# Performance work log

Measured on AMD Instinct MI355X. Metric: run time of the kernel, lower is better.

Reference implementation:

```python
import jax, jax.numpy as jnp
import numpy as np

LOG2 = 0.6931471805599453

def logcosh(x):
    # numerically stable log(cosh(x)) = |x| + log1p(exp(-2|x|)) - log(2)
    ax = jnp.abs(x)
    return ax + jnp.log1p(jnp.exp(-2.0 * ax)) - LOG2

def setup_inputs() -> dict:
    key = jax.random.key(0)
    k1, k2, k3 = jax.random.split(key, 3)
    B, N, G, F = 16384, 1024, 256, 16  # batch, n_sites, n_symm, alpha_symm
    # each row of perms is a valid permutation of [0, N)
    perms = jax.vmap(lambda k: jax.random.permutation(k, N))(jax.random.split(k1, G)).astype(jnp.int32)
    x = jax.random.normal(k2, (B, N), dtype=jnp.float32)
    W = jax.random.normal(k3, (N, F), dtype=jnp.float32) * 0.1  # kernel_init = normal(0.1)
    b = jnp.zeros((F,), dtype=jnp.float32)
    v_bias = jnp.zeros((1,), dtype=jnp.float32)
    return {"x": x, "W": W, "b": b, "v_bias": v_bias, "perms": perms}

def reference(x, W, b, v_bias, perms):
    # scan over group permutations: gather x by perm, matmul, bias, logcosh, sum
    def f(carry, perm):
        y = x[..., perm] @ W + b          # [B, F]
        return carry + jnp.sum(logcosh(y), axis=-1), None
    y0 = jnp.zeros(x.shape[:-1], dtype=x.dtype)
    y_out, _ = jax.lax.scan(f, y0, perms)
    y_out = y_out + v_bias[0] * jnp.sum(x, axis=-1)
    return y_out
```

## Files before the change

### kernel.cpp

```cpp
#include <hip/hip_runtime.h>
#include <math.h>

typedef __bf16 bf16x8 __attribute__((ext_vector_type(8)));
typedef float f32x4 __attribute__((ext_vector_type(4)));


__device__ __forceinline__ unsigned short f2bf(float f) {
    unsigned int u = __float_as_uint(f);
    u += 0x7FFFu + ((u >> 16) & 1u);
    return (unsigned short)(u >> 16);
}

__device__ __forceinline__ float logcosh_fast(float v) {
    float a = fabsf(v);
    float t = __expf(-2.0f * a);
    return a + (__logf(1.0f + t) - 0.6931471805599453f);
}

template <int CTRL>
__device__ __forceinline__ float dppadd(float x) {
    int y = __builtin_amdgcn_update_dpp(0, __float_as_int(x), CTRL, 0xf, 0xf, true);
    return x + __int_as_float(y);
}

__device__ __forceinline__ void gload_lds16(const void* g, void* l) {
    __builtin_amdgcn_global_load_lds(
        (__attribute__((address_space(1))) void*)(void*)g,
        (__attribute__((address_space(3))) void*)l, 16, 0, 0);
}

#define SBAR()  __builtin_amdgcn_s_barrier()
#define SCHED() __builtin_amdgcn_sched_barrier(0)

__global__ __launch_bounds__(256) void k_invert(const int* __restrict__ perms,
                                                int* __restrict__ inv) {
    int t = blockIdx.x * 256 + threadIdx.x;
    int g = t >> 10, n = t & 1023;
    inv[(g << 10) + perms[t]] = n;
}

__global__ __launch_bounds__(256) void k_build_bt(const float* __restrict__ W,
                                                  const int* __restrict__ inv,
                                                  unsigned short* __restrict__ bT) {
    int j = blockIdx.x;
    int g = j >> 4, f = j & 15;
    const int* invg = inv + (g << 10);
    size_t rowbase = (size_t)j << 10;
#pragma unroll
    for (int i = 0; i < 4; ++i) {
        int k = (i << 8) + threadIdx.x;
        int n = invg[k];
        bT[rowbase + k] = f2bf(W[(n << 4) + f]);
    }
}

__global__ __launch_bounds__(256) void k_convert(const float* __restrict__ x,
                                                 const float* __restrict__ vb,
                                                 unsigned short* __restrict__ xb,
                                                 float* __restrict__ out) {
    int row = blockIdx.x, tid = threadIdx.x;
    size_t base = ((size_t)row << 10) + (tid << 2);
    float4 v = *reinterpret_cast<const float4*>(x + base);
    ushort4 h;
    h.x = f2bf(v.x); h.y = f2bf(v.y); h.z = f2bf(v.z); h.w = f2bf(v.w);
    *reinterpret_cast<ushort4*>(xb + base) = h;
    float s = v.x + v.y + v.z + v.w;
#pragma unroll
    for (int off = 32; off > 0; off >>= 1) s += __shfl_down(s, off);
    __shared__ float ls[4];
    if ((tid & 63) == 0) ls[tid >> 6] = s;
    __syncthreads();
    if (tid == 0) out[row] = vb[0] * (ls[0] + ls[1] + ls[2] + ls[3]);
}


#define MFMA_QUAD(MH, NH)                                                        \
    _Pragma("unroll") for (int m_ = 0; m_ < 4; ++m_)                             \
    _Pragma("unroll") for (int n_ = 0; n_ < 2; ++n_)                             \
    _Pragma("unroll") for (int kk_ = 0; kk_ < 2; ++kk_)                          \
        acc[(MH) * 4 + m_][(NH) * 2 + n_] =                                      \
            __builtin_amdgcn_mfma_f32_16x16x32_bf16(                             \
                aF[(MH) * 4 + m_][kk_], bF[(NH) * 2 + n_][kk_],                  \
                acc[(MH) * 4 + m_][(NH) * 2 + n_], 0, 0, 0);

__global__ __launch_bounds__(512) void k_gemm(const unsigned short* __restrict__ xb,
                                              const unsigned short* __restrict__ bT,
                                              const float* __restrict__ bias,
                                              float* __restrict__ partial, int B) {
    __shared__ unsigned short As[2][256 * 64];
    __shared__ unsigned short Bs[2][256 * 64];

    const int tid = threadIdx.x;
    const int lane = tid & 63;
    const int wv = tid >> 6;
    const int wm = wv >> 2;
    const int wn = wv & 3;
    const int lr = lane & 15;
    const int lk = lane >> 4;

    const int fid = blockIdx.y * gridDim.x + blockIdx.x;
    const int cpx = (gridDim.x * gridDim.y) >> 3;
    const int swz = (fid & 7) * cpx + (fid >> 3);
    const int cbx = swz & 15;
    const int row0 = (swz >> 4) << 8;
    const int j0 = cbx << 8;

    const unsigned short* xbase = xb + ((size_t)row0 << 10);
    const unsigned short* bbase = bT + ((size_t)j0 << 10);

    const int aRow = (wm * 128 + lr) * 64;
    const int bRow = (wn * 64 + lr) * 64;
    const int po0 = (lk ^ (lr & 7)) * 8;
    const int po1 = ((4 + lk) ^ (lr & 7)) * 8;

    auto stage_half = [&](unsigned short* dst, const unsigned short* src, int h) {
#pragma unroll
        for (int j = 0; j < 2; ++j) {
            int c0 = (h * 128 + j * 64) * 8;
            int cc = c0 + tid;
            int r = cc >> 3;
            int cs = (cc & 7) ^ (r & 7);
            gload_lds16(src + (((size_t)r) << 10) + (cs << 3),
                        dst + ((c0 + wv * 64) << 3));
        }
    };
    auto stage_slot = [&](int tile, int part) {
        if (tile > 15) return;
        int p = tile & 1;
        const unsigned short* src = (part < 2 ? xbase : bbase) + (tile << 6);
        unsigned short* dst = (part < 2 ? &As[p][0] : &Bs[p][0]);
        stage_half(dst, src, part & 1);
    };

    f32x4 acc[8][4];
#pragma unroll
    for (int m = 0; m < 8; ++m)
#pragma unroll
        for (int n = 0; n < 4; ++n)
            acc[m][n] = {0.f, 0.f, 0.f, 0.f};

    stage_slot(0, 0); stage_slot(0, 1); stage_slot(0, 2); stage_slot(0, 3);
    stage_slot(1, 0);
    asm volatile("s_waitcnt vmcnt(2)" ::: "memory");
    SCHED();
    SBAR();

    for (int tt = 0; tt < 8; ++tt) {
        const int t = tt * 2;

        auto half_iter = [&](const unsigned short* Ap, const unsigned short* Bp,
                             int st1, int st4, int vm) {
            bf16x8 aF[8][2], bF[4][2];

#pragma unroll
            for (int m = 0; m < 4; ++m) {
                aF[m][0] = *reinterpret_cast<const bf16x8*>(Ap + aRow + po0 + m * 1024);
                aF[m][1] = *reinterpret_cast<const bf16x8*>(Ap + aRow + po1 + m * 1024);
            }
#pragma unroll
            for (int n = 0; n < 2; ++n) {
                bF[n][0] = *reinterpret_cast<const bf16x8*>(Bp + bRow + po0 + n * 1024);
                bF[n][1] = *reinterpret_cast<const bf16x8*>(Bp + bRow + po1 + n * 1024);
            }
            stage_slot(st1, 1);
            SCHED();
            SBAR();
            asm volatile("s_waitcnt lgkmcnt(0)" ::: "memory");
            SCHED();
            __builtin_amdgcn_s_setprio(1);
            MFMA_QUAD(0, 0)
            __builtin_amdgcn_s_setprio(0);
            SCHED();
            SBAR();

#pragma unroll
            for (int m = 4; m < 8; ++m) {
                aF[m][0] = *reinterpret_cast<const bf16x8*>(Ap + aRow + po0 + m * 1024);
                aF[m][1] = *reinterpret_cast<const bf16x8*>(Ap + aRow + po1 + m * 1024);
            }
            SCHED();
#pragma unroll
            for (int n = 2; n < 4; ++n) {
                bF[n][0] = *reinterpret_cast<const bf16x8*>(Bp + bRow + po0 + n * 1024);
                bF[n][1] = *reinterpret_cast<const bf16x8*>(Bp + bRow + po1 + n * 1024);
            }
            stage_slot(st1, 2);
            SCHED();
            SBAR();
            asm volatile("s_waitcnt lgkmcnt(4)" ::: "memory");
            SCHED();
            __builtin_amdgcn_s_setprio(1);
            MFMA_QUAD(1, 0)
            __builtin_amdgcn_s_setprio(0);
            SCHED();
            SBAR();

            stage_slot(st1, 3);
            SCHED();
            SBAR();
            asm volatile("s_waitcnt lgkmcnt(0)" ::: "memory");
            SCHED();
            __builtin_amdgcn_s_setprio(1);
            MFMA_QUAD(0, 1)
            __builtin_amdgcn_s_setprio(0);
            SCHED();
            SBAR();

            stage_slot(st4, 0);
            SCHED();
            SBAR();
            __builtin_amdgcn_s_setprio(1);
            MFMA_QUAD(1, 1)
            __builtin_amdgcn_s_setprio(0);
            SCHED();
            if (vm == 2)      { asm volatile("s_waitcnt vmcnt(2)" ::: "memory"); }
            else if (vm == 0) { asm volatile("s_waitcnt vmcnt(0)" ::: "memory"); }
            SCHED();
            SBAR();
        };

        half_iter(As[0], Bs[0], t + 1, t + 2, (tt < 7) ? 2 : 0);
        half_iter(As[1], Bs[1], t + 2, t + 3, (tt < 7) ? 2 : -1);
    }

    float* rowsum = (float*)&As[0][0];
    const float bv = bias[lr];
#pragma unroll
    for (int m = 0; m < 8; ++m) {
#pragma unroll
        for (int r = 0; r < 4; ++r) {
            float s = 0.f;
#pragma unroll
            for (int n = 0; n < 4; ++n) s += logcosh_fast(acc[m][n][r] + bv);
            s = dppadd<0x111>(s);
            s = dppadd<0x112>(s);
            s = dppadd<0x114>(s);
            s = dppadd<0x118>(s);
            if (lr == 15)
                rowsum[wn * 256 + wm * 128 + m * 16 + lk * 4 + r] = s;
        }
    }
    __syncthreads();
    if (tid < 256) {
        float s = rowsum[tid] + rowsum[256 + tid] + rowsum[512 + tid] + rowsum[768 + tid];
        partial[(size_t)cbx * B + row0 + tid] = s;
    }
}

__global__ __launch_bounds__(256) void k_final(const float* __restrict__ partial,
                                               float* __restrict__ out, int ncb, int B) {
    int b = blockIdx.x * 256 + threadIdx.x;
    float s = out[b];
    for (int c = 0; c < ncb; ++c) s += partial[(size_t)c * B + b];
    out[b] = s;
}

extern "C" void kernel_launch(void* const* d_in, const int* in_sizes, int n_in,
                              void* d_out, int out_size, void* d_ws, size_t ws_size,
                              hipStream_t stream) {
    const float* x      = (const float*)d_in[0];
    const float* W      = (const float*)d_in[1];
    const float* bias   = (const float*)d_in[2];
    const float* v_bias = (const float*)d_in[3];
    const int*   perms  = (const int*)d_in[4];
    float* out = (float*)d_out;

    const int N  = 1024;
    const int B  = in_sizes[0] / N;
    const int G  = in_sizes[4] / N;
    const int GF = G * 16;
    const int NCB = GF / 256;

    char* w = (char*)d_ws;
    unsigned short* xb = (unsigned short*)w;
    unsigned short* bT = (unsigned short*)(w + (size_t)B * N * 2);
    int* inv = (int*)(w + (size_t)B * N * 2 + (size_t)GF * N * 2);
    float* partial = (float*)(w + (size_t)B * N * 2 + (size_t)GF * N * 2
                              + (size_t)G * N * 4);

    k_invert<<<G * N / 256, 256, 0, stream>>>(perms, inv);
    k_build_bt<<<GF, 256, 0, stream>>>(W, inv, bT);
    k_convert<<<B, 256, 0, stream>>>(x, v_bias, xb, out);
    k_gemm<<<dim3(NCB, B / 256), 512, 0, stream>>>(xb, bT, bias, partial, B);
    k_final<<<B / 256, 256, 0, stream>>>(partial, out, NCB, B);
}
```

Baseline: 204.4 us.

## Restructure GEMM pipeline to prefetch next tile's fragments and reorder LDS staging

Replaces the lambda-based half-iteration with a templated tile4 step. It loads the next tile's first A/B register fragments at the end of the current tile, so the LDS reads overlap the last MFMA quadrant instead of stalling at the start. The staging schedule changes from A-ahead to a B-then-A order, and the prologue now preloads two A tiles. The launch bounds now ask for 2 blocks per CU, which pressures registers given the larger live fragment set and may cause spills. The risk is a race on LDS buffer reuse, since A is staged into the buffer currently being read.

```diff
diff --git a/kernel.cpp b/kernel.cpp
--- a/kernel.cpp
+++ b/kernel.cpp
@@ -83,10 +83,92 @@
                 aF[(MH) * 4 + m_][kk_], bF[(NH) * 2 + n_][kk_],                  \
                 acc[(MH) * 4 + m_][(NH) * 2 + n_], 0, 0, 0);
 
-__global__ __launch_bounds__(512) void k_gemm(const unsigned short* __restrict__ xb,
-                                              const unsigned short* __restrict__ bT,
-                                              const float* __restrict__ bias,
-                                              float* __restrict__ partial, int B) {
+__device__ __forceinline__ void stage_half(unsigned short* dst,
+                                           const unsigned short* src, int h,
+                                           int tid, int wv) {
+#pragma unroll
+    for (int j = 0; j < 2; ++j) {
+        int c0 = (h * 128 + j * 64) * 8;
+        int cc = c0 + tid;
+        int r = cc >> 3;
+        int cs = (cc & 7) ^ (r & 7);
+        gload_lds16(src + (((size_t)r) << 10) + (cs << 3),
+                    dst + ((c0 + wv * 64) << 3));
+    }
+}
+
+template <int VM, bool STB, bool STA, bool RDN>
+__device__ __forceinline__ void tile4(
+    const unsigned short* Ap, const unsigned short* Bp,
+    unsigned short* BsQ, unsigned short* AsP,
+    const unsigned short* bsrc, const unsigned short* xsrc,
+    const unsigned short* Aq, const unsigned short* Bq,
+    bf16x8 (&aF)[8][2], bf16x8 (&bF)[4][2], f32x4 (&acc)[8][4],
+    int aRow, int bRow, int po0, int po1, int tid, int wv) {
+#pragma unroll
+    for (int m = 4; m < 8; ++m) {
+        aF[m][0] = *reinterpret_cast<const bf16x8*>(Ap + aRow + po0 + m * 1024);
+        aF[m][1] = *reinterpret_cast<const bf16x8*>(Ap + aRow + po1 + m * 1024);
+    }
+    if (STB) stage_half(BsQ, bsrc, 0, tid, wv);
+    SCHED(); SBAR();
+    asm volatile("s_waitcnt lgkmcnt(8)" ::: "memory");
+    SCHED();
+    __builtin_amdgcn_s_setprio(1);
+    MFMA_QUAD(0, 0)
+    __builtin_amdgcn_s_setprio(0);
+    SCHED(); SBAR();
+
+#pragma unroll
+    for (int n = 2; n < 4; ++n) {
+        bF[n][0] = *reinterpret_cast<const bf16x8*>(Bp + bRow + po0 + n * 1024);
+        bF[n][1] = *reinterpret_cast<const bf16x8*>(Bp + bRow + po1 + n * 1024);
+    }
+    if (STB) stage_half(BsQ, bsrc, 1, tid, wv);
+    SCHED(); SBAR();
+    asm volatile("s_waitcnt lgkmcnt(4)" ::: "memory");
+    SCHED();
+    __builtin_amdgcn_s_setprio(1);
+    MFMA_QUAD(1, 0)
+    __builtin_amdgcn_s_setprio(0);
+    SCHED(); SBAR();
+
+    if (STA) stage_half(AsP, xsrc, 0, tid, wv);
+    SCHED(); SBAR();
+    asm volatile("s_waitcnt lgkmcnt(0)" ::: "memory");
+    SCHED();
+    __builtin_amdgcn_s_setprio(1);
+    MFMA_QUAD(0, 1)
+    __builtin_amdgcn_s_setprio(0);
+    SCHED();
+    if (VM == 2)      { asm volatile("s_waitcnt vmcnt(2)" ::: "memory"); }
+    else if (VM == 0) { asm volatile("s_waitcnt vmcnt(0)" ::: "memory"); }
+    SCHED(); SBAR();
+
+    if (RDN) {
+#pragma unroll
+        for (int m = 0; m < 4; ++m) {
+            aF[m][0] = *reinterpret_cast<const bf16x8*>(Aq + aRow + po0 + m * 1024);
+            aF[m][1] = *reinterpret_cast<const bf16x8*>(Aq + aRow + po1 + m * 1024);
+        }
+#pragma unroll
+        for (int n = 0; n < 2; ++n) {
+            bF[n][0] = *reinterpret_cast<const bf16x8*>(Bq + bRow + po0 + n * 1024);
+            bF[n][1] = *reinterpret_cast<const bf16x8*>(Bq + bRow + po1 + n * 1024);
+        }
+    }
+    if (STA) stage_half(AsP, xsrc, 1, tid, wv);
+    SCHED(); SBAR();
+    __builtin_amdgcn_s_setprio(1);
+    MFMA_QUAD(1, 1)
+    __builtin_amdgcn_s_setprio(0);
+    SCHED(); SBAR();
+}
+
+__global__ __launch_bounds__(512, 2) void k_gemm(const unsigned short* __restrict__ xb,
+                                                 const unsigned short* __restrict__ bT,
+                                                 const float* __restrict__ bias,
+                                                 float* __restrict__ partial, int B) {
     __shared__ unsigned short As[2][256 * 64];
     __shared__ unsigned short Bs[2][256 * 64];
 
@@ -113,25 +195,6 @@
     const int po0 = (lk ^ (lr & 7)) * 8;
     const int po1 = ((4 + lk) ^ (lr & 7)) * 8;
 
-    auto stage_half = [&](unsigned short* dst, const unsigned short* src, int h) {
-#pragma unroll
-        for (int j = 0; j < 2; ++j) {
-            int c0 = (h * 128 + j * 64) * 8;
-            int cc = c0 + tid;
-            int r = cc >> 3;
-            int cs = (cc & 7) ^ (r & 7);
-            gload_lds16(src + (((size_t)r) << 10) + (cs << 3),
-                        dst + ((c0 + wv * 64) << 3));
-        }
-    };
-    auto stage_slot = [&](int tile, int part) {
-        if (tile > 15) return;
-        int p = tile & 1;
-        const unsigned short* src = (part < 2 ? xbase : bbase) + (tile << 6);
-        unsigned short* dst = (part < 2 ? &As[p][0] : &Bs[p][0]);
-        stage_half(dst, src, part & 1);
-    };
-
     f32x4 acc[8][4];
 #pragma unroll
     for (int m = 0; m < 8; ++m)
@@ -139,89 +202,47 @@
         for (int n = 0; n < 4; ++n)
             acc[m][n] = {0.f, 0.f, 0.f, 0.f};
 
-    stage_slot(0, 0); stage_slot(0, 1); stage_slot(0, 2); stage_slot(0, 3);
-    stage_slot(1, 0);
-    asm volatile("s_waitcnt vmcnt(2)" ::: "memory");
-    SCHED();
-    SBAR();
-
-    for (int tt = 0; tt < 8; ++tt) {
-        const int t = tt * 2;
-
-        auto half_iter = [&](const unsigned short* Ap, const unsigned short* Bp,
-                             int st1, int st4, int vm) {
-            bf16x8 aF[8][2], bF[4][2];
-
-#pragma unroll
-            for (int m = 0; m < 4; ++m) {
-                aF[m][0] = *reinterpret_cast<const bf16x8*>(Ap + aRow + po0 + m * 1024);
-                aF[m][1] = *reinterpret_cast<const bf16x8*>(Ap + aRow + po1 + m * 1024);
-            }
-#pragma unroll
-            for (int n = 0; n < 2; ++n) {
-                bF[n][0] = *reinterpret_cast<const bf16x8*>(Bp + bRow + po0 + n * 1024);
-                bF[n][1] = *reinterpret_cast<const bf16x8*>(Bp + bRow + po1 + n * 1024);
-            }
-            stage_slot(st1, 1);
-            SCHED();
-            SBAR();
-            asm volatile("s_waitcnt lgkmcnt(0)" ::: "memory");
-            SCHED();
-            __builtin_amdgcn_s_setprio(1);
-            MFMA_QUAD(0, 0)
-            __builtin_amdgcn_s_setprio(0);
-            SCHED();
-            SBAR();
-
-#pragma unroll
-            for (int m = 4; m < 8; ++m) {
-                aF[m][0] = *reinterpret_cast<const bf16x8*>(Ap + aRow + po0 + m * 1024);
-                aF[m][1] = *reinterpret_cast<const bf16x8*>(Ap + aRow + po1 + m * 1024);
-            }
-            SCHED();
-#pragma unroll
-            for (int n = 2; n < 4; ++n) {
-                bF[n][0] = *reinterpret_cast<const bf16x8*>(Bp + bRow + po0 + n * 1024);
-                bF[n][1] = *reinterpret_cast<const bf16x8*>(Bp + bRow + po1 + n * 1024);
-            }
-            stage_slot(st1, 2);
-            SCHED();
-            SBAR();
-            asm volatile("s_waitcnt lgkmcnt(4)" ::: "memory");
-            SCHED();
-            __builtin_amdgcn_s_setprio(1);
-            MFMA_QUAD(1, 0)
-            __builtin_amdgcn_s_setprio(0);
-            SCHED();
-            SBAR();
-
-            stage_slot(st1, 3);
-            SCHED();
-            SBAR();
-            asm volatile("s_waitcnt lgkmcnt(0)" ::: "memory");
-            SCHED();
-            __builtin_amdgcn_s_setprio(1);
-            MFMA_QUAD(0, 1)
-            __builtin_amdgcn_s_setprio(0);
-            SCHED();
-            SBAR();
-
-            stage_slot(st4, 0);
-            SCHED();
-            SBAR();
-            __builtin_amdgcn_s_setprio(1);
-            MFMA_QUAD(1, 1)
-            __builtin_amdgcn_s_setprio(0);
-            SCHED();
-            if (vm == 2)      { asm volatile("s_waitcnt vmcnt(2)" ::: "memory"); }
-            else if (vm == 0) { asm volatile("s_waitcnt vmcnt(0)" ::: "memory"); }
-            SCHED();
-            SBAR();
-        };
-
-        half_iter(As[0], Bs[0], t + 1, t + 2, (tt < 7) ? 2 : 0);
-        half_iter(As[1], Bs[1], t + 2, t + 3, (tt < 7) ? 2 : -1);
-    }
+    bf16x8 aF[8][2], bF[4][2];
+
+    stage_half(&As[0][0], xbase, 0, tid, wv);
+    stage_half(&As[0][0], xbase, 1, tid, wv);
+    stage_half(&Bs[0][0], bbase, 0, tid, wv);
+    stage_half(&Bs[0][0], bbase, 1, tid, wv);
+    stage_half(&As[1][0], xbase + 64, 0, tid, wv);
+    stage_half(&As[1][0], xbase + 64, 1, tid, wv);
+    asm volatile("s_waitcnt vmcnt(4)" ::: "memory");
+    SCHED(); SBAR();
+#pragma unroll
+    for (int m = 0; m < 4; ++m) {
+        aF[m][0] = *reinterpret_cast<const bf16x8*>(&As[0][0] + aRow + po0 + m * 1024);
+        aF[m][1] = *reinterpret_cast<const bf16x8*>(&As[0][0] + aRow + po1 + m * 1024);
+    }
+#pragma unroll
+    for (int n = 0; n < 2; ++n) {
+        bF[n][0] = *reinterpret_cast<const bf16x8*>(&Bs[0][0] + bRow + po0 + n * 1024);
+        bF[n][1] = *reinterpret_cast<const bf16x8*>(&Bs[0][0] + bRow + po1 + n * 1024);
+    }
+    SCHED();
+
+    for (int tt = 0; tt < 7; ++tt) {
+        const int t0 = tt * 2;
+        tile4<2, true, true, true>(&As[0][0], &Bs[0][0], &Bs[1][0], &As[0][0],
+                                   bbase + ((t0 + 1) << 6), xbase + ((t0 + 2) << 6),
+                                   &As[1][0], &Bs[1][0],
+                                   aF, bF, acc, aRow, bRow, po0, po1, tid, wv);
+        tile4<2, true, true, true>(&As[1][0], &Bs[1][0], &Bs[0][0], &As[1][0],
+                                   bbase + ((t0 + 2) << 6), xbase + ((t0 + 3) << 6),
+                                   &As[0][0], &Bs[0][0],
+                                   aF, bF, acc, aRow, bRow, po0, po1, tid, wv);
+    }
+    tile4<0, true, false, true>(&As[0][0], &Bs[0][0], &Bs[1][0], &As[0][0],
+                                bbase + (15 << 6), xbase,
+                                &As[1][0], &Bs[1][0],
+                                aF, bF, acc, aRow, bRow, po0, po1, tid, wv);
+    tile4<-1, false, false, false>(&As[1][0], &Bs[1][0], &Bs[0][0], &As[1][0],
+                                   bbase, xbase,
+                                   &As[0][0], &Bs[0][0],
+                                   aF, bF, acc, aRow, bRow, po0, po1, tid, wv);
 
     float* rowsum = (float*)&As[0][0];
     const float bv = bias[lr];
```

Measured after the change: 250.9 us. +22.7%, slower.

## Restructure GEMM main loop into per-row MFMA pipeline with two-tile-ahead prefetch

Applied to the files above, without the earlier changes.

Replaces the quad-based half-iteration schedule with a tile iteration that loads all B fragments up front and streams A fragments one M-row at a time, interleaving LDS reads with MFMAs. Both double-buffer slots are now staged before the loop, and each tile refills its own slot two tiles ahead after its last LDS read, which cuts the number of barriers per tile. Launch bounds also request two blocks per CU. The tighter register budget from that hint could force spills of the large accumulator array, and LDS use may prevent the second block from fitting anyway.

```diff
diff --git a/kernel.cpp b/kernel.cpp
--- a/kernel.cpp
+++ b/kernel.cpp
@@ -74,19 +74,86 @@
 }
 
 
-#define MFMA_QUAD(MH, NH)                                                        \
-    _Pragma("unroll") for (int m_ = 0; m_ < 4; ++m_)                             \
-    _Pragma("unroll") for (int n_ = 0; n_ < 2; ++n_)                             \
-    _Pragma("unroll") for (int kk_ = 0; kk_ < 2; ++kk_)                          \
-        acc[(MH) * 4 + m_][(NH) * 2 + n_] =                                      \
-            __builtin_amdgcn_mfma_f32_16x16x32_bf16(                             \
-                aF[(MH) * 4 + m_][kk_], bF[(NH) * 2 + n_][kk_],                  \
-                acc[(MH) * 4 + m_][(NH) * 2 + n_], 0, 0, 0);
-
-__global__ __launch_bounds__(512) void k_gemm(const unsigned short* __restrict__ xb,
-                                              const unsigned short* __restrict__ bT,
-                                              const float* __restrict__ bias,
-                                              float* __restrict__ partial, int B) {
+#define MFMA_M(MM)                                                               \
+    _Pragma("unroll") for (int k_ = 0; k_ < 2; ++k_)                             \
+    _Pragma("unroll") for (int n_ = 0; n_ < 4; ++n_)                             \
+        acc[MM][n_] = __builtin_amdgcn_mfma_f32_16x16x32_bf16(                   \
+            aF[MM][k_], bF[n_][k_], acc[MM][n_], 0, 0, 0);
+
+__device__ __forceinline__ void stage_half(unsigned short* dst,
+                                           const unsigned short* src, int h,
+                                           int tid, int wv) {
+#pragma unroll
+    for (int j = 0; j < 2; ++j) {
+        int c0 = (h * 128 + j * 64) * 8;
+        int cc = c0 + tid;
+        int r = cc >> 3;
+        int cs = (cc & 7) ^ (r & 7);
+        gload_lds16(src + (((size_t)r) << 10) + (cs << 3),
+                    dst + ((c0 + wv * 64) << 3));
+    }
+}
+
+template <bool STAGE, int VM>
+__device__ __forceinline__ void tile_iter(
+    const unsigned short* Ap, const unsigned short* Bp,
+    unsigned short* AsD, unsigned short* BsD,
+    const unsigned short* xsrc, const unsigned short* bsrc,
+    f32x4 (&acc)[8][4], int aRow, int bRow, int po0, int po1, int tid, int wv) {
+    bf16x8 aF[8][2], bF[4][2];
+
+#pragma unroll
+    for (int n = 0; n < 4; ++n) {
+        bF[n][0] = *reinterpret_cast<const bf16x8*>(Bp + bRow + po0 + n * 1024);
+        bF[n][1] = *reinterpret_cast<const bf16x8*>(Bp + bRow + po1 + n * 1024);
+    }
+#pragma unroll
+    for (int m = 0; m < 2; ++m) {
+        aF[m][0] = *reinterpret_cast<const bf16x8*>(Ap + aRow + po0 + m * 1024);
+        aF[m][1] = *reinterpret_cast<const bf16x8*>(Ap + aRow + po1 + m * 1024);
+    }
+    SCHED();
+
+#pragma unroll
+    for (int m = 0; m < 6; ++m) {
+        aF[m + 2][0] = *reinterpret_cast<const bf16x8*>(Ap + aRow + po0 + (m + 2) * 1024);
+        aF[m + 2][1] = *reinterpret_cast<const bf16x8*>(Ap + aRow + po1 + (m + 2) * 1024);
+        SCHED();
+        asm volatile("s_waitcnt lgkmcnt(4)" ::: "memory");
+        SCHED();
+        __builtin_amdgcn_s_setprio(1);
+        MFMA_M(m)
+        __builtin_amdgcn_s_setprio(0);
+        SCHED();
+    }
+
+    asm volatile("s_waitcnt lgkmcnt(0)" ::: "memory");
+    SCHED();
+    SBAR();
+
+    if (STAGE) { stage_half(AsD, xsrc, 0, tid, wv); stage_half(AsD, xsrc, 1, tid, wv); }
+    SCHED();
+    __builtin_amdgcn_s_setprio(1);
+    MFMA_M(6)
+    __builtin_amdgcn_s_setprio(0);
+    SCHED();
+
+    if (STAGE) { stage_half(BsD, bsrc, 0, tid, wv); stage_half(BsD, bsrc, 1, tid, wv); }
+    SCHED();
+    __builtin_amdgcn_s_setprio(1);
+    MFMA_M(7)
+    __builtin_amdgcn_s_setprio(0);
+    SCHED();
+    if (VM == 8)      { asm volatile("s_waitcnt vmcnt(8)" ::: "memory"); }
+    else if (VM == 0) { asm volatile("s_waitcnt vmcnt(0)" ::: "memory"); }
+    SCHED();
+    SBAR();
+}
+
+__global__ __launch_bounds__(512, 2) void k_gemm(const unsigned short* __restrict__ xb,
+                                                 const unsigned short* __restrict__ bT,
+                                                 const float* __restrict__ bias,
+                                                 float* __restrict__ partial, int B) {
     __shared__ unsigned short As[2][256 * 64];
     __shared__ unsigned short Bs[2][256 * 64];
 
@@ -113,25 +180,6 @@
     const int po0 = (lk ^ (lr & 7)) * 8;
     const int po1 = ((4 + lk) ^ (lr & 7)) * 8;
 
-    auto stage_half = [&](unsigned short* dst, const unsigned short* src, int h) {
-#pragma unroll
-        for (int j = 0; j < 2; ++j) {
-            int c0 = (h * 128 + j * 64) * 8;
-            int cc = c0 + tid;
-            int r = cc >> 3;
-            int cs = (cc & 7) ^ (r & 7);
-            gload_lds16(src + (((size_t)r) << 10) + (cs << 3),
-                        dst + ((c0 + wv * 64) << 3));
-        }
-    };
-    auto stage_slot = [&](int tile, int part) {
-        if (tile > 15) return;
-        int p = tile & 1;
-        const unsigned short* src = (part < 2 ? xbase : bbase) + (tile << 6);
-        unsigned short* dst = (part < 2 ? &As[p][0] : &Bs[p][0]);
-        stage_half(dst, src, part & 1);
-    };
-
     f32x4 acc[8][4];
 #pragma unroll
     for (int m = 0; m < 8; ++m)
@@ -139,89 +187,31 @@
         for (int n = 0; n < 4; ++n)
             acc[m][n] = {0.f, 0.f, 0.f, 0.f};
 
-    stage_slot(0, 0); stage_slot(0, 1); stage_slot(0, 2); stage_slot(0, 3);
-    stage_slot(1, 0);
-    asm volatile("s_waitcnt vmcnt(2)" ::: "memory");
+    stage_half(&As[0][0], xbase, 0, tid, wv);
+    stage_half(&As[0][0], xbase, 1, tid, wv);
+    stage_half(&Bs[0][0], bbase, 0, tid, wv);
+    stage_half(&Bs[0][0], bbase, 1, tid, wv);
+    stage_half(&As[1][0], xbase + 64, 0, tid, wv);
+    stage_half(&As[1][0], xbase + 64, 1, tid, wv);
+    stage_half(&Bs[1][0], bbase + 64, 0, tid, wv);
+    stage_half(&Bs[1][0], bbase + 64, 1, tid, wv);
+    asm volatile("s_waitcnt vmcnt(8)" ::: "memory");
     SCHED();
     SBAR();
 
-    for (int tt = 0; tt < 8; ++tt) {
-        const int t = tt * 2;
-
-        auto half_iter = [&](const unsigned short* Ap, const unsigned short* Bp,
-                             int st1, int st4, int vm) {
-            bf16x8 aF[8][2], bF[4][2];
-
-#pragma unroll
-            for (int m = 0; m < 4; ++m) {
-                aF[m][0] = *reinterpret_cast<const bf16x8*>(Ap + aRow + po0 + m * 1024);
-                aF[m][1] = *reinterpret_cast<const bf16x8*>(Ap + aRow + po1 + m * 1024);
-            }
-#pragma unroll
-            for (int n = 0; n < 2; ++n) {
-                bF[n][0] = *reinterpret_cast<const bf16x8*>(Bp + bRow + po0 + n * 1024);
-                bF[n][1] = *reinterpret_cast<const bf16x8*>(Bp + bRow + po1 + n * 1024);
-            }
-            stage_slot(st1, 1);
-            SCHED();
-            SBAR();
-            asm volatile("s_waitcnt lgkmcnt(0)" ::: "memory");
-            SCHED();
-            __builtin_amdgcn_s_setprio(1);
-            MFMA_QUAD(0, 0)
-            __builtin_amdgcn_s_setprio(0);
-            SCHED();
-            SBAR();
-
-#pragma unroll
-            for (int m = 4; m < 8; ++m) {
-                aF[m][0] = *reinterpret_cast<const bf16x8*>(Ap + aRow + po0 + m * 1024);
-                aF[m][1] = *reinterpret_cast<const bf16x8*>(Ap + aRow + po1 + m * 1024);
-            }
-            SCHED();
-#pragma unroll
-            for (int n = 2; n < 4; ++n) {
-                bF[n][0] = *reinterpret_cast<const bf16x8*>(Bp + bRow + po0 + n * 1024);
-                bF[n][1] = *reinterpret_cast<const bf16x8*>(Bp + bRow + po1 + n * 1024);
-            }
-            stage_slot(st1, 2);
-            SCHED();
-            SBAR();
-            asm volatile("s_waitcnt lgkmcnt(4)" ::: "memory");
-            SCHED();
-            __builtin_amdgcn_s_setprio(1);
-            MFMA_QUAD(1, 0)
-            __builtin_amdgcn_s_setprio(0);
-            SCHED();
-            SBAR();
-
-            stage_slot(st1, 3);
-            SCHED();
-            SBAR();
-            asm volatile("s_waitcnt lgkmcnt(0)" ::: "memory");
-            SCHED();
-            __builtin_amdgcn_s_setprio(1);
-            MFMA_QUAD(0, 1)
-            __builtin_amdgcn_s_setprio(0);
-            SCHED();
-            SBAR();
-
-            stage_slot(st4, 0);
-            SCHED();
-            SBAR();
-            __builtin_amdgcn_s_setprio(1);
-            MFMA_QUAD(1, 1)
-            __builtin_amdgcn_s_setprio(0);
-            SCHED();
-            if (vm == 2)      { asm volatile("s_waitcnt vmcnt(2)" ::: "memory"); }
-            else if (vm == 0) { asm volatile("s_waitcnt vmcnt(0)" ::: "memory"); }
-            SCHED();
-            SBAR();
-        };
-
-        half_iter(As[0], Bs[0], t + 1, t + 2, (tt < 7) ? 2 : 0);
-        half_iter(As[1], Bs[1], t + 2, t + 3, (tt < 7) ? 2 : -1);
-    }
+    for (int tt = 0; tt < 7; ++tt) {
+        const int t0 = tt * 2;
+        tile_iter<true, 8>(&As[0][0], &Bs[0][0], &As[0][0], &Bs[0][0],
+                           xbase + ((t0 + 2) << 6), bbase + ((t0 + 2) << 6),
+                           acc, aRow, bRow, po0, po1, tid, wv);
+        tile_iter<true, 8>(&As[1][0], &Bs[1][0], &As[1][0], &Bs[1][0],
+                           xbase + ((t0 + 3) << 6), bbase + ((t0 + 3) << 6),
+                           acc, aRow, bRow, po0, po1, tid, wv);
+    }
+    tile_iter<false, 0>(&As[0][0], &Bs[0][0], &As[0][0], &Bs[0][0],
+                        xbase, bbase, acc, aRow, bRow, po0, po1, tid, wv);
+    tile_iter<false, -1>(&As[1][0], &Bs[1][0], &As[1][0], &Bs[1][0],
+                         xbase, bbase, acc, aRow, bRow, po0, po1, tid, wv);
 
     float* rowsum = (float*)&As[0][0];
     const float bv = bias[lr];
```

After: 188.4 us. 1.08x faster.
